# Kernel tuning notes

Measured on AMD Instinct MI355X. Metric: run time of the kernel, lower is better.

The kernel has to match this reference:

```python
import jax, jax.numpy as jnp
import numpy as np

B, L, H, E, V = 8, 8192, 512, 256, 8192  # L == V required by the pointer-gen mixing line


def setup_inputs() -> dict:
    key = jax.random.key(0)
    ks = jax.random.split(key, 20)
    f = lambda k, shape, sc=0.05: jax.random.normal(k, shape, jnp.float32) * sc
    # torch LSTM bias init: zeros, with forget-gate slice [n//4:n//2] set to 1 (applied to both b_ih and b_hh)
    lstm_bias = jnp.concatenate([jnp.zeros(H), jnp.ones(H), jnp.zeros(2 * H)]).astype(jnp.float32)
    return {
        'h': f(ks[0], (B, L, 2 * H), 1.0),
        's_h': f(ks[1], (B, H), 1.0),
        's_c': f(ks[2], (B, H), 1.0),
        'y_t_prev': jax.random.randint(ks[3], (B,), 0, V),
        'c_t_pre': f(ks[4], (B, 2 * H), 1.0),
        'coverage': jnp.zeros((B, L), jnp.float32),
        'emb': f(ks[5], (V, E)),
        'feed_W': f(ks[6], (E, E + 2 * H)),
        'feed_b': f(ks[7], (E,)),
        'Wih': f(ks[8], (4 * H, E)),
        'Whh': f(ks[9], (4 * H, H)),
        'bih': lstm_bias,
        'bhh': lstm_bias,
        'attn_W': f(ks[10], (2 * H, 4 * H + 1)),
        'attn_b': f(ks[11], (2 * H,)),
        'attn_v': f(ks[12], (2 * H,)),
        'pgen_W': f(ks[13], (4 * H + E,)),
        'pgen_b': f(ks[14], (1,)),
        'V_W': f(ks[15], (H, 3 * H)),
        'V_b': f(ks[16], (H,)),
        'Vp_W': f(ks[17], (V, H)),
        'Vp_b': f(ks[18], (V,)),
    }


def reference(h, s_h, s_c, y_t_prev, c_t_pre, coverage, emb, feed_W, feed_b,
              Wih, Whh, bih, bhh, attn_W, attn_b, attn_v, pgen_W, pgen_b,
              V_W, V_b, Vp_W, Vp_b):
    # --- input feeding ---
    x = emb[y_t_prev]                                             # (B, E)
    x = jnp.concatenate([x, c_t_pre], axis=-1) @ feed_W.T + feed_b  # (B, E)
    # --- single LSTM step (torch gate order: i, f, g, o) ---
    gates = x @ Wih.T + bih + s_h @ Whh.T + bhh                    # (B, 4H)
    i, fg, g, o = jnp.split(gates, 4, axis=-1)
    c_new = jax.nn.sigmoid(fg) * s_c + jax.nn.sigmoid(i) * jnp.tanh(g)
    h_new = jax.nn.sigmoid(o) * jnp.tanh(c_new)                    # s_t_tilde (B, H)
    s_hat = jnp.concatenate([h_new, c_new], axis=-1)               # (B, 2H)
    # --- additive attention with coverage (concat->linear split into 3 terms) ---
    Wh = attn_W[:, :2 * H]          # applied to encoder states h
    Ws = attn_W[:, 2 * H:4 * H]     # applied to decoder state s_hat
    wc = attn_W[:, 4 * H]           # applied to coverage scalar, (2H,)
    feat = jnp.tanh(jnp.einsum('bln,mn->blm', h, Wh)
                    + (s_hat @ Ws.T)[:, None, :]
                    + coverage[..., None] * wc
                    + attn_b)                                      # (B, L, 2H)
    scores = feat @ attn_v                                         # (B, L)
    attn = jax.nn.softmax(scores, axis=-1)
    c_t = jnp.einsum('bl,bln->bn', attn, h)                        # (B, 2H)
    coverage_next = coverage + attn
    # --- pointer-generator gate ---
    p_gen = jax.nn.sigmoid(jnp.concatenate([c_t, s_hat, x], axis=-1) @ pgen_W + pgen_b)[:, None]  # (B, 1)
    p_gen = p_gen[:, 0, :] if p_gen.ndim == 3 else p_gen
    # --- vocab distribution ---
    logits = (jnp.concatenate([h_new, c_t], axis=-1) @ V_W.T + V_b) @ Vp_W.T + Vp_b  # (B, V)
    P_vocab = jax.nn.softmax(logits, axis=-1)
    P_w = p_gen * P_vocab + (1.0 - p_gen) * attn                   # requires L == V
    return P_w, attn, c_t, coverage_next, h_new, c_new, p_gen
```

## Files before the change

kernel.cpp:

```cpp
#include <hip/hip_runtime.h>
#include <hip/hip_bf16.h>
#include <math.h>


#define MTOT 65536

typedef __attribute__((ext_vector_type(8))) short bf16x8;
typedef __attribute__((ext_vector_type(4))) float f32x4;
typedef unsigned int u32;

__device__ __forceinline__ float sigf(float x) { return 1.0f / (1.0f + expf(-x)); }
__device__ __forceinline__ float wave_sum(float v) {
    v += __shfl_xor(v, 1);  v += __shfl_xor(v, 2);  v += __shfl_xor(v, 4);
    v += __shfl_xor(v, 8);  v += __shfl_xor(v, 16); v += __shfl_xor(v, 32);
    return v;
}
__device__ __forceinline__ unsigned short f2bu(float f) {
    union { float f; unsigned int i; } c; c.f = f;
    unsigned int x = c.i;
    return (unsigned short)((x + 0x7fffu + ((x >> 16) & 1u)) >> 16);
}
__device__ __forceinline__ void gl16(const void* g, void* l) {
    __builtin_amdgcn_global_load_lds(
        (const __attribute__((address_space(1))) u32*)g,
        (__attribute__((address_space(3))) u32*)l, 16, 0, 0);
}

__global__ void wh_kernel(const float* __restrict__ attn_W, const float* __restrict__ attn_v,
                          unsigned short* __restrict__ Whx,
                          float* __restrict__ wcf, float* __restrict__ avf) {
    int tid = threadIdx.x;
    int idx0 = blockIdx.x * 1024 + tid * 4;
    #pragma unroll
    for (int t = 0; t < 4; ++t) {
        int idx = idx0 + t;
        int m = idx >> 10, n = idx & 1023;
        Whx[idx] = f2bu(attn_W[(size_t)m * 2049 + n]);
    }
    if (blockIdx.x == 0) {
        for (int i = tid; i < 1024; i += 256) {
            wcf[i] = attn_W[(size_t)i * 2049 + 2048];
            avf[i] = attn_v[i];
        }
    }
}

__global__ void feed_kernel(const int* __restrict__ y_prev, const float* __restrict__ emb,
                            const float* __restrict__ c_t_pre,
                            const float* __restrict__ feed_W,
                            const float* __restrict__ feed_b, float* __restrict__ xo) {
    __shared__ float cat[8 * 1280];
    int tid = threadIdx.x;
    for (int idx = tid; idx < 8 * 1280; idx += 256) {
        int b = idx / 1280, k = idx - b * 1280;
        cat[idx] = (k < 256) ? emb[(size_t)y_prev[b] * 256 + k]
                             : c_t_pre[b * 1024 + (k - 256)];
    }
    __syncthreads();
    int e = blockIdx.x * 4 + (tid >> 6);
    int lane = tid & 63;
    float acc[8] = {};
    for (int k = lane; k < 1280; k += 64) {
        float w = feed_W[(size_t)e * 1280 + k];
        #pragma unroll
        for (int b = 0; b < 8; ++b) acc[b] += w * cat[b * 1280 + k];
    }
    #pragma unroll
    for (int b = 0; b < 8; ++b) acc[b] = wave_sum(acc[b]);
    if (lane == 0) {
        float fb = feed_b[e];
        #pragma unroll
        for (int b = 0; b < 8; ++b) xo[b * 256 + e] = acc[b] + fb;
    }
}

__global__ void gates_kernel(const float* __restrict__ x, const float* __restrict__ s_h,
                             const float* __restrict__ Wih, const float* __restrict__ Whh,
                             const float* __restrict__ bih, const float* __restrict__ bhh,
                             float* __restrict__ gates) {
    __shared__ float xs[8 * 256];
    __shared__ float hs[8 * 512];
    int tid = threadIdx.x;
    for (int i = tid; i < 2048; i += 256) xs[i] = x[i];
    for (int i = tid; i < 4096; i += 256) hs[i] = s_h[i];
    __syncthreads();
    int j = blockIdx.x * 4 + (tid >> 6);
    int lane = tid & 63;
    float acc[8] = {};
    for (int k = lane; k < 256; k += 64) {
        float w = Wih[(size_t)j * 256 + k];
        #pragma unroll
        for (int b = 0; b < 8; ++b) acc[b] += w * xs[b * 256 + k];
    }
    for (int k = lane; k < 512; k += 64) {
        float w = Whh[(size_t)j * 512 + k];
        #pragma unroll
        for (int b = 0; b < 8; ++b) acc[b] += w * hs[b * 512 + k];
    }
    #pragma unroll
    for (int b = 0; b < 8; ++b) acc[b] = wave_sum(acc[b]);
    if (lane == 0) {
        float bb = bih[j] + bhh[j];
        #pragma unroll
        for (int b = 0; b < 8; ++b) gates[b * 2048 + j] = acc[b] + bb;
    }
}

__global__ void lstm_kernel(const float* __restrict__ gates, const float* __restrict__ s_c,
                            float* __restrict__ out_h, float* __restrict__ out_c,
                            float* __restrict__ shat) {
    int idx = blockIdx.x * 256 + threadIdx.x;
    int b = idx >> 9, u = idx & 511;
    const float* g = gates + b * 2048;
    float ig = sigf(g[u]), fg = sigf(g[512 + u]), gg = tanhf(g[1024 + u]), og = sigf(g[1536 + u]);
    float c = fg * s_c[idx] + ig * gg;
    float h = og * tanhf(c);
    out_h[idx] = h;
    out_c[idx] = c;
    shat[b * 1024 + u] = h;
    shat[b * 1024 + 512 + u] = c;
}

__global__ void sterm_kernel(const float* __restrict__ shat, const float* __restrict__ attn_W,
                             const float* __restrict__ attn_b, float* __restrict__ sterm) {
    __shared__ float ss[8 * 1024];
    int tid = threadIdx.x;
    for (int i = tid; i < 8192; i += 256) ss[i] = shat[i];
    __syncthreads();
    int m = blockIdx.x * 4 + (tid >> 6);
    int lane = tid & 63;
    float acc[8] = {};
    for (int k = lane; k < 1024; k += 64) {
        float w = attn_W[(size_t)m * 2049 + 1024 + k];
        #pragma unroll
        for (int b = 0; b < 8; ++b) acc[b] += w * ss[b * 1024 + k];
    }
    #pragma unroll
    for (int b = 0; b < 8; ++b) acc[b] = wave_sum(acc[b]);
    if (lane == 0) {
        float ab = attn_b[m];
        #pragma unroll
        for (int b = 0; b < 8; ++b) sterm[b * 1024 + m] = acc[b] + ab;
    }
}

__global__ __launch_bounds__(256, 3)
void attn_gemm_kernel(const float* __restrict__ h, const unsigned short* __restrict__ Whx,
                      const float* __restrict__ sterm, const float* __restrict__ coverage,
                      const float* __restrict__ wcf, const float* __restrict__ avf,
                      float* __restrict__ scores_part) {
    __shared__ uint4 As4[2048];
    __shared__ uint4 Bs4[1024];
    char* As = (char*)As4;
    char* Bs = (char*)Bs4;
    int tid = threadIdx.x;
    int id = blockIdx.x;
    int ct = (id >> 3) & 7;
    int rt = (id & 7) + ((id >> 6) << 3);
    int r0 = rt * 128, m0 = ct * 128;
    int lane = tid & 63, wid = tid >> 6;
    int wr = wid >> 1, wc = wid & 1;
    f32x4 acc[4][4] = {};

    int lrowB = lane >> 3;
    int lsrcB = (lane & 7) ^ lrowB;
    int rA7  = (wid * 4 + (lane >> 4)) & 7;
    int srcA = ((((lane & 15) >> 1) ^ rA7) << 3) + ((lane & 1) << 2);

    for (int t = 0; t < 16; ++t) {
        int k0 = t * 64;
        const float* hA = h + (size_t)r0 * 1024 + k0;
        const unsigned short* wB = Whx + (size_t)m0 * 1024 + k0;
        #pragma unroll
        for (int i = 0; i < 8; ++i) {
            int row = i * 16 + wid * 4 + (lane >> 4);
            gl16(hA + (size_t)row * 1024 + srcA, As + i * 4096 + wid * 1024);
        }
        #pragma unroll
        for (int i = 0; i < 4; ++i) {
            int row = i * 32 + wid * 8 + lrowB;
            gl16(wB + (size_t)row * 1024 + lsrcB * 8, Bs + i * 4096 + wid * 1024);
        }
        __syncthreads();

        #pragma unroll
        for (int kh = 0; kh < 2; ++kh) {
            int cb = kh * 4 + (lane >> 4);
            bf16x8 af[4], bfr[4];
            #pragma unroll
            for (int mi = 0; mi < 4; ++mi) {
                int row = wr * 64 + mi * 16 + (lane & 15);
                int pc = (cb ^ (row & 7)) << 5;
                uint4 lo = *reinterpret_cast<const uint4*>(As + row * 256 + pc);
                uint4 hi = *reinterpret_cast<const uint4*>(As + row * 256 + pc + 16);
                uint4 pk;
                pk.x = __builtin_amdgcn_perm(lo.y, lo.x, 0x07060302u);
                pk.y = __builtin_amdgcn_perm(lo.w, lo.z, 0x07060302u);
                pk.z = __builtin_amdgcn_perm(hi.y, hi.x, 0x07060302u);
                pk.w = __builtin_amdgcn_perm(hi.w, hi.z, 0x07060302u);
                af[mi] = *reinterpret_cast<bf16x8*>(&pk);
            }
            #pragma unroll
            for (int ni = 0; ni < 4; ++ni) {
                int row = wc * 64 + ni * 16 + (lane & 15);
                bfr[ni] = *reinterpret_cast<const bf16x8*>(Bs + row * 128 + ((cb ^ (row & 7)) << 4));
            }
            #pragma unroll
            for (int mi = 0; mi < 4; ++mi)
                #pragma unroll
                for (int ni = 0; ni < 4; ++ni)
                    acc[mi][ni] = __builtin_amdgcn_mfma_f32_16x16x32_bf16(af[mi], bfr[ni], acc[mi][ni], 0, 0, 0);
        }
        __syncthreads();
    }

    float* red = (float*)As4;
    int b = r0 >> 13;
    float covv[4][4];
    #pragma unroll
    for (int mi = 0; mi < 4; ++mi)
        #pragma unroll
        for (int j = 0; j < 4; ++j)
            covv[mi][j] = coverage[r0 + wr * 64 + mi * 16 + ((lane >> 4) << 2) + j];
    float rs[4][4] = {};
    #pragma unroll
    for (int ni = 0; ni < 4; ++ni) {
        int m = m0 + wc * 64 + ni * 16 + (lane & 15);
        float stm = sterm[b * 1024 + m];
        float wcm = wcf[m], avm = avf[m];
        #pragma unroll
        for (int mi = 0; mi < 4; ++mi)
            #pragma unroll
            for (int j = 0; j < 4; ++j) {
                float val = acc[mi][ni][j] + stm + covv[mi][j] * wcm;
                rs[mi][j] += tanhf(val) * avm;
            }
    }
    #pragma unroll
    for (int mi = 0; mi < 4; ++mi)
        #pragma unroll
        for (int j = 0; j < 4; ++j) {
            float v = rs[mi][j];
            v += __shfl_xor(v, 1); v += __shfl_xor(v, 2);
            v += __shfl_xor(v, 4); v += __shfl_xor(v, 8);
            rs[mi][j] = v;
        }
    __syncthreads();
    if ((lane & 15) == 0) {
        int g4 = lane >> 4;
        #pragma unroll
        for (int mi = 0; mi < 4; ++mi)
            #pragma unroll
            for (int j = 0; j < 4; ++j)
                red[(wr * 64 + mi * 16 + g4 * 4 + j) * 2 + wc] = rs[mi][j];
    }
    __syncthreads();
    if (tid < 128)
        scores_part[(size_t)ct * MTOT + r0 + tid] = red[tid * 2] + red[tid * 2 + 1];
}

__global__ void softmax_cov_kernel(const float* __restrict__ scores_part,
                                   const float* __restrict__ coverage,
                                   float* __restrict__ attn_out,
                                   float* __restrict__ cov_out,
                                   float* __restrict__ attnf) {
    __shared__ float s[8192];
    __shared__ float wred[16];
    int b = blockIdx.x, tid = threadIdx.x;
    int lane = tid & 63, wid = tid >> 6;
    float lmax = -1e30f;
    for (int l = tid; l < 8192; l += 1024) {
        float v = 0.f;
        #pragma unroll
        for (int p = 0; p < 8; ++p) v += scores_part[(size_t)p * MTOT + b * 8192 + l];
        s[l] = v;
        lmax = fmaxf(lmax, v);
    }
    #pragma unroll
    for (int o = 32; o; o >>= 1) lmax = fmaxf(lmax, __shfl_xor(lmax, o));
    if (lane == 0) wred[wid] = lmax;
    __syncthreads();
    float bmax = wred[0];
    #pragma unroll
    for (int i = 1; i < 16; ++i) bmax = fmaxf(bmax, wred[i]);
    float lsum = 0.f;
    for (int l = tid; l < 8192; l += 1024) {
        float e = expf(s[l] - bmax);
        s[l] = e;
        lsum += e;
    }
    lsum = wave_sum(lsum);
    __syncthreads();
    if (lane == 0) wred[wid] = lsum;
    __syncthreads();
    float tsum = 0.f;
    #pragma unroll
    for (int i = 0; i < 16; ++i) tsum += wred[i];
    float inv = 1.0f / tsum;
    for (int l = tid; l < 8192; l += 1024) {
        float a = s[l] * inv;
        attnf[b * 8192 + l] = a;
        attn_out[b * 8192 + l] = a;
        cov_out[b * 8192 + l] = coverage[b * 8192 + l] + a;
    }
}

__global__ void ct_partial_kernel(const float* __restrict__ h,
                                  const float* __restrict__ attnf, float* __restrict__ ct_part) {
    int blk = blockIdx.x;
    int b = blk >> 6, ch = blk & 63;
    int tid = threadIdx.x;
    float a0 = 0, a1 = 0, a2 = 0, a3 = 0;
    int rbase = b * 8192 + ch * 128;
    for (int l = 0; l < 128; ++l) {
        float a = attnf[rbase + l];
        float4 hv = *reinterpret_cast<const float4*>(h + (size_t)(rbase + l) * 1024 + tid * 4);
        a0 += a * hv.x; a1 += a * hv.y; a2 += a * hv.z; a3 += a * hv.w;
    }
    float4 o; o.x = a0; o.y = a1; o.z = a2; o.w = a3;
    *reinterpret_cast<float4*>(ct_part + (size_t)blk * 1024 + tid * 4) = o;
}

__global__ void ct_reduce_kernel(const float* __restrict__ ct_part, float* __restrict__ ctf,
                                 float* __restrict__ ct_out) {
    int idx = blockIdx.x * 256 + threadIdx.x;
    int b = idx >> 10, n = idx & 1023;
    const float* p = ct_part + (size_t)b * 64 * 1024 + n;
    float s = 0.f;
    #pragma unroll 8
    for (int c = 0; c < 64; ++c) s += p[c * 1024];
    ctf[idx] = s;
    ct_out[idx] = s;
}

__global__ void u_kernel(const float* __restrict__ shat, const float* __restrict__ ctf,
                         const float* __restrict__ V_W, const float* __restrict__ V_b,
                         float* __restrict__ u) {
    __shared__ float cat[8 * 1536];
    int tid = threadIdx.x;
    for (int idx = tid; idx < 8 * 1536; idx += 256) {
        int b = idx / 1536, k = idx - b * 1536;
        cat[idx] = (k < 512) ? shat[b * 1024 + k] : ctf[b * 1024 + (k - 512)];
    }
    __syncthreads();
    int i = blockIdx.x * 4 + (tid >> 6);
    int lane = tid & 63;
    float acc[8] = {};
    for (int k = lane; k < 1536; k += 64) {
        float w = V_W[(size_t)i * 1536 + k];
        #pragma unroll
        for (int b = 0; b < 8; ++b) acc[b] += w * cat[b * 1536 + k];
    }
    #pragma unroll
    for (int b = 0; b < 8; ++b) acc[b] = wave_sum(acc[b]);
    if (lane == 0) {
        float vb = V_b[i];
        #pragma unroll
        for (int b = 0; b < 8; ++b) u[b * 512 + i] = acc[b] + vb;
    }
}

__global__ void pgen_kernel(const float* __restrict__ ctf, const float* __restrict__ shat,
                            const float* __restrict__ x, const float* __restrict__ pgen_W,
                            const float* __restrict__ pgen_b,
                            float* __restrict__ pgenf, float* __restrict__ pgen_out) {
    int tid = threadIdx.x;
    int b = tid >> 6, lane = tid & 63;
    float acc = 0.f;
    for (int k = lane; k < 2304; k += 64) {
        float v;
        if (k < 1024)      v = ctf[b * 1024 + k];
        else if (k < 2048) v = shat[b * 1024 + (k - 1024)];
        else               v = x[b * 256 + (k - 2048)];
        acc += pgen_W[k] * v;
    }
    acc = wave_sum(acc);
    if (lane == 0) {
        float p = sigf(acc + pgen_b[0]);
        pgenf[b] = p;
        pgen_out[b] = p;
    }
}

__global__ void logits_kernel(const float* __restrict__ u, const float* __restrict__ Vp_W,
                              const float* __restrict__ Vp_b, float* __restrict__ logits) {
    __shared__ float us[8 * 512];
    int tid = threadIdx.x;
    for (int i = tid; i < 4096; i += 256) us[i] = u[i];
    __syncthreads();
    int v = blockIdx.x * 4 + (tid >> 6);
    int lane = tid & 63;
    float acc[8] = {};
    for (int k = lane; k < 512; k += 64) {
        float w = Vp_W[(size_t)v * 512 + k];
        #pragma unroll
        for (int b = 0; b < 8; ++b) acc[b] += w * us[b * 512 + k];
    }
    #pragma unroll
    for (int b = 0; b < 8; ++b) acc[b] = wave_sum(acc[b]);
    if (lane == 0) {
        float vb = Vp_b[v];
        #pragma unroll
        for (int b = 0; b < 8; ++b) logits[b * 8192 + v] = acc[b] + vb;
    }
}

__global__ void final_kernel(const float* __restrict__ logits, const float* __restrict__ pgenf,
                             const float* __restrict__ attnf, float* __restrict__ pw_out) {
    __shared__ float s[8192];
    __shared__ float wred[16];
    int b = blockIdx.x, tid = threadIdx.x;
    int lane = tid & 63, wid = tid >> 6;
    float lmax = -1e30f;
    for (int l = tid; l < 8192; l += 1024) {
        float v = logits[b * 8192 + l];
        s[l] = v;
        lmax = fmaxf(lmax, v);
    }
    #pragma unroll
    for (int o = 32; o; o >>= 1) lmax = fmaxf(lmax, __shfl_xor(lmax, o));
    if (lane == 0) wred[wid] = lmax;
    __syncthreads();
    float bmax = wred[0];
    #pragma unroll
    for (int i = 1; i < 16; ++i) bmax = fmaxf(bmax, wred[i]);
    float lsum = 0.f;
    for (int l = tid; l < 8192; l += 1024) {
        float e = expf(s[l] - bmax);
        s[l] = e;
        lsum += e;
    }
    lsum = wave_sum(lsum);
    __syncthreads();
    if (lane == 0) wred[wid] = lsum;
    __syncthreads();
    float tsum = 0.f;
    #pragma unroll
    for (int i = 0; i < 16; ++i) tsum += wred[i];
    float inv = 1.0f / tsum;
    float pg = pgenf[b];
    for (int l = tid; l < 8192; l += 1024) {
        float pv = s[l] * inv;
        pw_out[b * 8192 + l] = pg * pv + (1.0f - pg) * attnf[b * 8192 + l];
    }
}

extern "C" void kernel_launch(void* const* d_in, const int* in_sizes, int n_in,
                              void* d_out, int out_size, void* d_ws, size_t ws_size,
                              hipStream_t stream) {
    (void)in_sizes; (void)n_in; (void)out_size; (void)ws_size;
    const float* h        = (const float*)d_in[0];
    const float* s_h      = (const float*)d_in[1];
    const float* s_c      = (const float*)d_in[2];
    const int*   y_prev   = (const int*)d_in[3];
    const float* c_t_pre  = (const float*)d_in[4];
    const float* coverage = (const float*)d_in[5];
    const float* emb      = (const float*)d_in[6];
    const float* feed_W   = (const float*)d_in[7];
    const float* feed_b   = (const float*)d_in[8];
    const float* Wih      = (const float*)d_in[9];
    const float* Whh      = (const float*)d_in[10];
    const float* bih      = (const float*)d_in[11];
    const float* bhh      = (const float*)d_in[12];
    const float* attn_W   = (const float*)d_in[13];
    const float* attn_b   = (const float*)d_in[14];
    const float* attn_v   = (const float*)d_in[15];
    const float* pgen_W   = (const float*)d_in[16];
    const float* pgen_b   = (const float*)d_in[17];
    const float* V_W      = (const float*)d_in[18];
    const float* V_b      = (const float*)d_in[19];
    const float* Vp_W     = (const float*)d_in[20];
    const float* Vp_b     = (const float*)d_in[21];

    float* out    = (float*)d_out;
    float* o_pw   = out;
    float* o_attn = out + 65536;
    float* o_ct   = out + 131072;
    float* o_cov  = out + 139264;
    float* o_hnew = out + 204800;
    float* o_cnew = out + 208896;
    float* o_pgen = out + 212992;

    float* ws = (float*)d_ws;
    float* ws_x       = ws;
    float* ws_gates   = ws + 2048;
    float* ws_shat    = ws + 18432;
    float* ws_sterm   = ws + 26624;
    float* ws_u       = ws + 34816;
    float* ws_logits  = ws + 38912;
    float* ws_pgen    = ws + 104448;
    float* ws_wc      = ws + 105472;
    float* ws_av      = ws + 106496;
    float* ws_attnf   = ws + 107520;
    float* ws_scoresp = ws + 173056;
    float* ws_ctpart  = ws + 697344;
    float* ws_ctf     = ws + 1221632;
    unsigned short* ws_whx = (unsigned short*)(ws + 1229824);

    wh_kernel<<<1024, 256, 0, stream>>>(attn_W, attn_v, ws_whx, ws_wc, ws_av);
    feed_kernel<<<64, 256, 0, stream>>>(y_prev, emb, c_t_pre, feed_W, feed_b, ws_x);
    gates_kernel<<<512, 256, 0, stream>>>(ws_x, s_h, Wih, Whh, bih, bhh, ws_gates);
    lstm_kernel<<<16, 256, 0, stream>>>(ws_gates, s_c, o_hnew, o_cnew, ws_shat);
    sterm_kernel<<<256, 256, 0, stream>>>(ws_shat, attn_W, attn_b, ws_sterm);
    attn_gemm_kernel<<<4096, 256, 0, stream>>>(h, ws_whx, ws_sterm, coverage,
                                               ws_wc, ws_av, ws_scoresp);
    softmax_cov_kernel<<<8, 1024, 0, stream>>>(ws_scoresp, coverage, o_attn, o_cov, ws_attnf);
    ct_partial_kernel<<<512, 256, 0, stream>>>(h, ws_attnf, ws_ctpart);
    ct_reduce_kernel<<<32, 256, 0, stream>>>(ws_ctpart, ws_ctf, o_ct);
    u_kernel<<<128, 256, 0, stream>>>(ws_shat, ws_ctf, V_W, V_b, ws_u);
    pgen_kernel<<<1, 512, 0, stream>>>(ws_ctf, ws_shat, ws_x, pgen_W, pgen_b, ws_pgen, o_pgen);
    logits_kernel<<<2048, 256, 0, stream>>>(ws_u, Vp_W, Vp_b, ws_logits);
    final_kernel<<<8, 1024, 0, stream>>>(ws_logits, ws_pgen, ws_attnf, o_pw);
}
```

Before: 374.9 us.

## Triple-buffer attention GEMM LDS tiles with async prefetch two stages ahead

Converts the attention-score GEMM main loop from a single-buffered load-sync-compute pattern to a three-stage LDS ring. Global-to-LDS loads run two K-tiles ahead, with a partial vmcnt wait and one barrier per iteration. The goal is to hide global memory latency behind the MFMA work. LDS use grows to 144 KB per block, so launch bounds drop to one block per CU, which reduces occupancy.

New measurement: 667.2 us. 1.78x slower.

```diff
diff --git a/kernel.cpp b/kernel.cpp
--- a/kernel.cpp
+++ b/kernel.cpp
@@ -144,15 +144,13 @@
     }
 }
 
-__global__ __launch_bounds__(256, 3)
+__global__ __launch_bounds__(256, 1)
 void attn_gemm_kernel(const float* __restrict__ h, const unsigned short* __restrict__ Whx,
                       const float* __restrict__ sterm, const float* __restrict__ coverage,
                       const float* __restrict__ wcf, const float* __restrict__ avf,
                       float* __restrict__ scores_part) {
-    __shared__ uint4 As4[2048];
-    __shared__ uint4 Bs4[1024];
-    char* As = (char*)As4;
-    char* Bs = (char*)Bs4;
+    __shared__ uint4 As4[3][2048];
+    __shared__ uint4 Bs4[3][1024];
     int tid = threadIdx.x;
     int id = blockIdx.x;
     int ct = (id >> 3) & 7;
@@ -167,22 +165,37 @@
     int rA7  = (wid * 4 + (lane >> 4)) & 7;
     int srcA = ((((lane & 15) >> 1) ^ rA7) << 3) + ((lane & 1) << 2);
 
-    for (int t = 0; t < 16; ++t) {
-        int k0 = t * 64;
-        const float* hA = h + (size_t)r0 * 1024 + k0;
-        const unsigned short* wB = Whx + (size_t)m0 * 1024 + k0;
+    const float* hbase = h + (size_t)r0 * 1024;
+    const unsigned short* wbase = Whx + (size_t)m0 * 1024;
+
+    auto STAGE = [&](int tt, int bb) {
+        int k0 = tt * 64;
+        char* As = (char*)As4[bb];
+        char* Bs = (char*)Bs4[bb];
         #pragma unroll
         for (int i = 0; i < 8; ++i) {
             int row = i * 16 + wid * 4 + (lane >> 4);
-            gl16(hA + (size_t)row * 1024 + srcA, As + i * 4096 + wid * 1024);
+            gl16(hbase + (size_t)row * 1024 + k0 + srcA, As + i * 4096 + wid * 1024);
         }
         #pragma unroll
         for (int i = 0; i < 4; ++i) {
             int row = i * 32 + wid * 8 + lrowB;
-            gl16(wB + (size_t)row * 1024 + lsrcB * 8, Bs + i * 4096 + wid * 1024);
+            gl16(wbase + (size_t)row * 1024 + k0 + lsrcB * 8, Bs + i * 4096 + wid * 1024);
         }
-        __syncthreads();
-
+    };
+
+    STAGE(0, 0);
+    STAGE(1, 1);
+
+    for (int t = 0; t < 16; ++t) {
+        if (t < 15) asm volatile("s_waitcnt vmcnt(12)" ::: "memory");
+        else        asm volatile("s_waitcnt vmcnt(0)"  ::: "memory");
+        __builtin_amdgcn_s_barrier();
+        __builtin_amdgcn_sched_barrier(0);
+        if (t + 2 < 16) STAGE(t + 2, (t + 2) % 3);
+
+        const char* As = (const char*)As4[t % 3];
+        const char* Bs = (const char*)Bs4[t % 3];
         #pragma unroll
         for (int kh = 0; kh < 2; ++kh) {
             int cb = kh * 4 + (lane >> 4);
@@ -211,7 +224,6 @@
                 for (int ni = 0; ni < 4; ++ni)
                     acc[mi][ni] = __builtin_amdgcn_mfma_f32_16x16x32_bf16(af[mi], bfr[ni], acc[mi][ni], 0, 0, 0);
         }
-        __syncthreads();
     }
 
     float* red = (float*)As4;
```
